# Kernel tuning notes

Measured on AMD Instinct MI355X. Metric: run time of the kernel, lower is better.

## Reference

```python
import jax, jax.numpy as jnp
import numpy as np

NUM_STEPS = 5


def setup_inputs() -> dict:
    key = jax.random.key(0)
    ks = jax.random.split(key, 12)
    B, N, H, E, A = 8, 1024, 64, 2, 8
    initial_state = jax.random.normal(ks[0], (B, N, H), dtype=jnp.float32)
    annotation = jax.random.normal(ks[1], (B, N, A), dtype=jnp.float32)
    # sparse-ish positive adjacency, scaled so matmul outputs don't saturate gates
    adj_matrix = jax.random.uniform(ks[2], (B, N, 2 * N * E), dtype=jnp.float32) * 0.01
    s = 0.05
    W_edge = jax.random.normal(ks[3], (H, H * E), dtype=jnp.float32) * s
    b_edge = jax.random.normal(ks[4], (H * E,), dtype=jnp.float32) * s
    W_gate = jax.random.normal(ks[5], (3 * H, H), dtype=jnp.float32) * s
    b_gate = jax.random.normal(ks[6], (H,), dtype=jnp.float32) * s
    W_hid = jax.random.normal(ks[7], (H + A, H), dtype=jnp.float32) * s
    b_hid = jax.random.normal(ks[8], (H,), dtype=jnp.float32) * s
    W_out = jax.random.normal(ks[9], (H, 1), dtype=jnp.float32) * s
    b_out = jax.random.normal(ks[10], (1,), dtype=jnp.float32) * s
    return dict(initial_state=initial_state, annotation=annotation, adj_matrix=adj_matrix,
                W_edge=W_edge, b_edge=b_edge, W_gate=W_gate, b_gate=b_gate,
                W_hid=W_hid, b_hid=b_hid, W_out=W_out, b_out=b_out)


def reference(initial_state, annotation, adj_matrix, W_edge, b_edge,
              W_gate, b_gate, W_hid, b_hid, W_out, b_out):
    B, N, H = initial_state.shape
    E = W_edge.shape[1] // H
    boundary = N * E
    A_in = adj_matrix[:, :, :boundary]   # [B, N, N*E]
    A_out = adj_matrix[:, :, boundary:]  # [B, N, N*E]

    h = initial_state
    for _ in range(NUM_STEPS):
        # Linear(H, H*E) then view/transpose to [B, N*E, H].
        # Original computes incoming_edge and outgoing_edge with the SAME
        # linear on the SAME input -> identical tensors; compute once.
        edge = jnp.einsum('bnh,he->bne', h, W_edge) + b_edge      # [B, N, H*E]
        edge = edge.reshape(B, N, H, E).transpose(0, 3, 1, 2).reshape(B, N * E, H)
        a_in = jnp.matmul(A_in, edge)    # [B, N, H]
        a_out = jnp.matmul(A_out, edge)  # [B, N, H]
        a = jnp.concatenate([a_in, a_out, h], axis=2)             # [B, N, 3H]
        # update and reset use the same gate linear -> equal; compute once.
        z = jax.nn.sigmoid(jnp.einsum('bnk,kh->bnh', a, W_gate) + b_gate)
        a_r = jnp.concatenate([a_in, a_out, z * h], axis=2)
        h_tilde = jnp.tanh(jnp.einsum('bnk,kh->bnh', a_r, W_gate) + b_gate)
        h = (1.0 - z) * h + z * h_tilde

    # task_id not in {18, 19}: node-level output head
    ha = jnp.concatenate([h, annotation], axis=2)                 # [B, N, H+A]
    out = jnp.tanh(jnp.einsum('bnk,kh->bnh', ha, W_hid) + b_hid)  # [B, N, H]
    out = (jnp.einsum('bnh,ho->bno', out, W_out) + b_out).sum(axis=2)  # [B, N]
    return out
```

## Files before the change

### kernel.cpp

```cpp
#include <hip/hip_runtime.h>
#include <math.h>

#define BN    8
#define NN    1024
#define HH    64
#define ADIM  8
#define STEPS 5
#define K2    2048
#define ROWS  (BN*NN)

typedef __attribute__((ext_vector_type(8))) short bf16x8;
typedef __attribute__((ext_vector_type(4))) float f32x4;

__device__ __forceinline__ unsigned short f2bf(float f) {
    unsigned int u = __float_as_uint(f);
    u += 0x7FFF + ((u >> 16) & 1);
    return (unsigned short)(u >> 16);
}
__device__ __forceinline__ float bf2f(unsigned short h) {
    return __uint_as_float(((unsigned int)h) << 16);
}

__global__ __launch_bounds__(256) void conv_adj(
    const float* __restrict__ in, unsigned short* __restrict__ out)
{
    int tid = blockIdx.x * 256 + threadIdx.x;
    #pragma unroll
    for (int i = 0; i < 4; ++i) {
        size_t idx = (size_t)tid + (size_t)i * 2097152;
        float4 v = ((const float4*)in)[idx];
        ushort4 o;
        o.x = f2bf(v.x); o.y = f2bf(v.y); o.z = f2bf(v.z); o.w = f2bf(v.w);
        ((ushort4*)out)[idx] = o;
    }
}

__global__ __launch_bounds__(256) void prep_pack(
    const float* __restrict__ Wg, const float* __restrict__ We,
    unsigned short* __restrict__ wgp, unsigned short* __restrict__ wep)
{
    int t = blockIdx.x * 256 + threadIdx.x;
    if (t < 12288) {
        int k = t >> 6, c = t & 63;
        float v = Wg[t];
        unsigned short hi = f2bf(v);
        unsigned short lo = f2bf(v - bf2f(hi));
        wgp[(size_t)c * 192 + k] = hi;
        wgp[(size_t)(64 + c) * 192 + k] = lo;
    } else if (t < 20480) {
        int u = t - 12288;
        int k = u >> 7, c = u & 127;
        float v = We[u];
        unsigned short hi = f2bf(v);
        unsigned short lo = f2bf(v - bf2f(hi));
        wep[(size_t)c * 64 + k] = hi;
        wep[(size_t)(128 + c) * 64 + k] = lo;
    }
}

__global__ __launch_bounds__(256) void init_kernel(
    const float* __restrict__ init_state,
    const float* __restrict__ We, const float* __restrict__ be,
    float* __restrict__ h_ws, unsigned short* __restrict__ edge_t)
{
    __shared__ float h_lds[4][65];
    int t = threadIdx.x;
    int r = t >> 6, hp = t & 63;
    int row = blockIdx.x * 4 + r;
    float hv = init_state[(size_t)row * 64 + hp];
    h_ws[(size_t)row * 64 + hp] = hv;
    h_lds[r][hp] = hv;
    __syncthreads();
    int b = row >> 10, n = row & 1023;
    #pragma unroll
    for (int e = 0; e < 2; ++e) {
        float acc = be[hp * 2 + e];
        #pragma unroll 8
        for (int c = 0; c < 64; ++c)
            acc += h_lds[r][c] * We[c * 128 + hp * 2 + e];
        edge_t[((size_t)b * 64 + hp) * K2 + e * NN + n] = f2bf(acc);
    }
}

__global__ __launch_bounds__(256) void step_kernel(
    const unsigned short* __restrict__ adjb,
    const unsigned short* __restrict__ ein,
    unsigned short* __restrict__ eout,
    float* __restrict__ h_ws,
    const unsigned short* __restrict__ wgp,
    const unsigned short* __restrict__ wep,
    const float* __restrict__ bg,
    const float* __restrict__ be,
    int do_edge)
{
    __shared__ __attribute__((aligned(16))) unsigned short Bs[2][64][264];
    __shared__ __attribute__((aligned(16))) unsigned short Xhi[32][200];
    __shared__ __attribute__((aligned(16))) unsigned short Xlo[32][200];
    __shared__ __attribute__((aligned(16))) float          hf [32][68];
    __shared__ __attribute__((aligned(16))) unsigned short HNhi[32][72];
    __shared__ __attribute__((aligned(16))) unsigned short HNlo[32][72];

    int t  = threadIdx.x;
    int b  = blockIdx.x >> 5;
    int mt = blockIdx.x & 31;
    int n0 = mt * 32;
    size_t hbase = ((size_t)(b * NN + n0)) * 64;

    {
        int r = t >> 3, cg = (t & 7) * 8;
        const float* hptr = h_ws + hbase + (size_t)r * 64 + cg;
        float4 v0 = *(const float4*)hptr;
        float4 v1 = *(const float4*)(hptr + 4);
        float vv[8] = {v0.x, v0.y, v0.z, v0.w, v1.x, v1.y, v1.z, v1.w};
        #pragma unroll
        for (int j = 0; j < 8; ++j) {
            float v = vv[j];
            unsigned short hi = f2bf(v), lo = f2bf(v - bf2f(hi));
            Xhi[r][128 + cg + j] = hi;
            Xlo[r][128 + cg + j] = lo;
            hf[r][cg + j] = v;
        }
    }

    int lane = t & 63, w = t >> 6, l15 = lane & 15, q = lane >> 4;
    int dir = w >> 1, rh = w & 1;

    const unsigned short* Abase = adjb
        + ((size_t)(b * NN + n0 + rh * 16 + l15)) * 4096 + dir * K2;

    int srow[8], scol[8];
    const unsigned short* sptr[8];
    #pragma unroll
    for (int i = 0; i < 8; ++i) {
        int u = i * 256 + t;
        srow[i] = u >> 5; scol[i] = (u & 31) * 8;
        sptr[i] = ein + ((size_t)b * 64 + srow[i]) * K2 + scol[i];
    }
    #pragma unroll
    for (int i = 0; i < 8; ++i)
        *(uint4*)&Bs[0][srow[i]][scol[i]] = *(const uint4*)(sptr[i]);
    __syncthreads();

    f32x4 acc[4];
    #pragma unroll
    for (int ct = 0; ct < 4; ++ct) acc[ct] = (f32x4){0.f, 0.f, 0.f, 0.f};

    bf16x8 af[8];
    #pragma unroll
    for (int ks = 0; ks < 8; ++ks)
        af[ks] = *(const bf16x8*)(Abase + ks * 32 + q * 8);

    #pragma unroll
    for (int c = 0; c < 8; ++c) {
        int buf = c & 1;
        uint4 g[8];
        bf16x8 afn[8];
        if (c < 7) {
            #pragma unroll
            for (int i = 0; i < 8; ++i)
                g[i] = *(const uint4*)(sptr[i] + (c + 1) * 256);
            #pragma unroll
            for (int ks = 0; ks < 8; ++ks)
                afn[ks] = *(const bf16x8*)(Abase + (c + 1) * 256 + ks * 32 + q * 8);
        }
        #pragma unroll
        for (int ks = 0; ks < 8; ++ks) {
            #pragma unroll
            for (int ct = 0; ct < 4; ++ct) {
                bf16x8 bfr = *(const bf16x8*)&Bs[buf][ct * 16 + l15][ks * 32 + q * 8];
                acc[ct] = __builtin_amdgcn_mfma_f32_16x16x32_bf16(af[ks], bfr, acc[ct], 0, 0, 0);
            }
        }
        if (c < 7) {
            #pragma unroll
            for (int i = 0; i < 8; ++i)
                *(uint4*)&Bs[buf ^ 1][srow[i]][scol[i]] = g[i];
            #pragma unroll
            for (int ks = 0; ks < 8; ++ks) af[ks] = afn[ks];
        }
        __syncthreads();
    }

    #pragma unroll
    for (int ct = 0; ct < 4; ++ct) {
        #pragma unroll
        for (int i = 0; i < 4; ++i) {
            float v = acc[ct][i];
            unsigned short hi = f2bf(v), lo = f2bf(v - bf2f(hi));
            int r  = rh * 16 + q * 4 + i;
            int cc = dir * 64 + ct * 16 + l15;
            Xhi[r][cc] = hi;
            Xlo[r][cc] = lo;
        }
    }
    __syncthreads();

    int mg = w & 1, ct0 = (w >> 1) * 2;
    int arow = mg * 16 + l15;
    f32x4 as[2], az[2];
    as[0] = as[1] = (f32x4){0.f, 0.f, 0.f, 0.f};

    #pragma unroll
    for (int ks = 0; ks < 4; ++ks) {
        bf16x8 ah = *(const bf16x8*)&Xhi[arow][ks * 32 + q * 8];
        bf16x8 al = *(const bf16x8*)&Xlo[arow][ks * 32 + q * 8];
        #pragma unroll
        for (int p = 0; p < 2; ++p) {
            int cc = (ct0 + p) * 16 + l15;
            const unsigned short* wb = wgp + (size_t)cc * 192 + ks * 32 + q * 8;
            bf16x8 bh = *(const bf16x8*)wb;
            bf16x8 bl = *(const bf16x8*)(wb + 64 * 192);
            as[p] = __builtin_amdgcn_mfma_f32_16x16x32_bf16(ah, bh, as[p], 0, 0, 0);
            as[p] = __builtin_amdgcn_mfma_f32_16x16x32_bf16(ah, bl, as[p], 0, 0, 0);
            as[p] = __builtin_amdgcn_mfma_f32_16x16x32_bf16(al, bh, as[p], 0, 0, 0);
        }
    }
    az[0] = as[0]; az[1] = as[1];
    #pragma unroll
    for (int ks = 4; ks < 6; ++ks) {
        bf16x8 ah = *(const bf16x8*)&Xhi[arow][ks * 32 + q * 8];
        bf16x8 al = *(const bf16x8*)&Xlo[arow][ks * 32 + q * 8];
        #pragma unroll
        for (int p = 0; p < 2; ++p) {
            int cc = (ct0 + p) * 16 + l15;
            const unsigned short* wb = wgp + (size_t)cc * 192 + ks * 32 + q * 8;
            bf16x8 bh = *(const bf16x8*)wb;
            bf16x8 bl = *(const bf16x8*)(wb + 64 * 192);
            az[p] = __builtin_amdgcn_mfma_f32_16x16x32_bf16(ah, bh, az[p], 0, 0, 0);
            az[p] = __builtin_amdgcn_mfma_f32_16x16x32_bf16(ah, bl, az[p], 0, 0, 0);
            az[p] = __builtin_amdgcn_mfma_f32_16x16x32_bf16(al, bh, az[p], 0, 0, 0);
        }
    }
    __syncthreads();

    float zv[2][4], hv[2][4];
    #pragma unroll
    for (int p = 0; p < 2; ++p) {
        int cc = (ct0 + p) * 16 + l15;
        float bgv = bg[cc];
        #pragma unroll
        for (int i = 0; i < 4; ++i) {
            int r = mg * 16 + q * 4 + i;
            float z = 1.f / (1.f + __expf(-(az[p][i] + bgv)));
            float h = hf[r][cc];
            zv[p][i] = z; hv[p][i] = h;
            float zh = z * h;
            unsigned short hi = f2bf(zh), lo = f2bf(zh - bf2f(hi));
            Xhi[r][128 + cc] = hi;
            Xlo[r][128 + cc] = lo;
        }
    }
    __syncthreads();

    #pragma unroll
    for (int ks = 4; ks < 6; ++ks) {
        bf16x8 ah = *(const bf16x8*)&Xhi[arow][ks * 32 + q * 8];
        bf16x8 al = *(const bf16x8*)&Xlo[arow][ks * 32 + q * 8];
        #pragma unroll
        for (int p = 0; p < 2; ++p) {
            int cc = (ct0 + p) * 16 + l15;
            const unsigned short* wb = wgp + (size_t)cc * 192 + ks * 32 + q * 8;
            bf16x8 bh = *(const bf16x8*)wb;
            bf16x8 bl = *(const bf16x8*)(wb + 64 * 192);
            as[p] = __builtin_amdgcn_mfma_f32_16x16x32_bf16(ah, bh, as[p], 0, 0, 0);
            as[p] = __builtin_amdgcn_mfma_f32_16x16x32_bf16(ah, bl, as[p], 0, 0, 0);
            as[p] = __builtin_amdgcn_mfma_f32_16x16x32_bf16(al, bh, as[p], 0, 0, 0);
        }
    }

    #pragma unroll
    for (int p = 0; p < 2; ++p) {
        int cc = (ct0 + p) * 16 + l15;
        float bgv = bg[cc];
        #pragma unroll
        for (int i = 0; i < 4; ++i) {
            int r = mg * 16 + q * 4 + i;
            float ht = tanhf(as[p][i] + bgv);
            float z  = zv[p][i];
            float hn = (1.f - z) * hv[p][i] + z * ht;
            h_ws[hbase + (size_t)r * 64 + cc] = hn;
            if (do_edge) {
                unsigned short hi = f2bf(hn), lo = f2bf(hn - bf2f(hi));
                HNhi[r][cc] = hi;
                HNlo[r][cc] = lo;
            }
        }
    }
    if (!do_edge) return;
    __syncthreads();

    int me = w & 1, cb = (w >> 1) * 4;
    int erow = me * 16 + l15;
    f32x4 ae[4];
    #pragma unroll
    for (int p = 0; p < 4; ++p) ae[p] = (f32x4){0.f, 0.f, 0.f, 0.f};
    #pragma unroll
    for (int ks = 0; ks < 2; ++ks) {
        bf16x8 ah = *(const bf16x8*)&HNhi[erow][ks * 32 + q * 8];
        bf16x8 al = *(const bf16x8*)&HNlo[erow][ks * 32 + q * 8];
        #pragma unroll
        for (int p = 0; p < 4; ++p) {
            int cc = (cb + p) * 16 + l15;
            const unsigned short* wb = wep + (size_t)cc * 64 + ks * 32 + q * 8;
            bf16x8 bh = *(const bf16x8*)wb;
            bf16x8 bl = *(const bf16x8*)(wb + 128 * 64);
            ae[p] = __builtin_amdgcn_mfma_f32_16x16x32_bf16(ah, bh, ae[p], 0, 0, 0);
            ae[p] = __builtin_amdgcn_mfma_f32_16x16x32_bf16(ah, bl, ae[p], 0, 0, 0);
            ae[p] = __builtin_amdgcn_mfma_f32_16x16x32_bf16(al, bh, ae[p], 0, 0, 0);
        }
    }
    #pragma unroll
    for (int p = 0; p < 4; ++p) {
        int cc = (cb + p) * 16 + l15;
        float bev = be[cc];
        int hp2 = cc >> 1, e = cc & 1;
        size_t ebase = ((size_t)b * 64 + hp2) * K2 + (size_t)e * NN
                     + n0 + me * 16 + q * 4;
        ushort4 ev;
        ev.x = f2bf(ae[p][0] + bev);
        ev.y = f2bf(ae[p][1] + bev);
        ev.z = f2bf(ae[p][2] + bev);
        ev.w = f2bf(ae[p][3] + bev);
        *(ushort4*)(eout + ebase) = ev;
    }
}

__global__ __launch_bounds__(256) void head_kernel(
    const float* __restrict__ h_ws, const float* __restrict__ ann,
    const float* __restrict__ Wh, const float* __restrict__ bh,
    const float* __restrict__ Wo, const float* __restrict__ bo,
    float* __restrict__ out)
{
    __shared__ float Wh_l[72 * 64];
    __shared__ float ha[4][72];
    int t = threadIdx.x;
    #pragma unroll
    for (int l = 0; l < 18; ++l) {
        int idx = t + l * 256;
        Wh_l[idx] = Wh[idx];
    }
    int r = t >> 6, hp = t & 63;
    int row = blockIdx.x * 4 + r;
    ha[r][hp] = h_ws[(size_t)row * 64 + hp];
    if (hp < ADIM) ha[r][64 + hp] = ann[(size_t)row * ADIM + hp];
    __syncthreads();

    float acc = bh[hp];
    #pragma unroll 8
    for (int k = 0; k < 72; ++k)
        acc += ha[r][k] * Wh_l[k * 64 + hp];
    float v = tanhf(acc) * Wo[hp];
    #pragma unroll
    for (int o = 32; o; o >>= 1) v += __shfl_down(v, o, 64);
    if (hp == 0) out[row] = v + bo[0];
}

extern "C" void kernel_launch(void* const* d_in, const int* in_sizes, int n_in,
                              void* d_out, int out_size, void* d_ws, size_t ws_size,
                              hipStream_t stream) {
    const float* init_state = (const float*)d_in[0];
    const float* ann = (const float*)d_in[1];
    const float* adj = (const float*)d_in[2];
    const float* We  = (const float*)d_in[3];
    const float* be  = (const float*)d_in[4];
    const float* Wg  = (const float*)d_in[5];
    const float* bg  = (const float*)d_in[6];
    const float* Wh  = (const float*)d_in[7];
    const float* bh  = (const float*)d_in[8];
    const float* Wo  = (const float*)d_in[9];
    const float* bo  = (const float*)d_in[10];
    float* out = (float*)d_out;

    char* wsb = (char*)d_ws;
    unsigned short* adj_bf = (unsigned short*)wsb;
    unsigned short* edge_a = (unsigned short*)(wsb + 67108864);
    unsigned short* edge_b = (unsigned short*)(wsb + 69206016);
    float*          h_ws   = (float*)(wsb + 71303168);
    unsigned short* wgp    = (unsigned short*)(wsb + 73400320);
    unsigned short* wep    = (unsigned short*)(wsb + 73449472);

    conv_adj<<<dim3(8192), dim3(256), 0, stream>>>(adj, adj_bf);
    prep_pack<<<dim3(80), dim3(256), 0, stream>>>(Wg, We, wgp, wep);
    init_kernel<<<dim3(ROWS / 4), dim3(256), 0, stream>>>(init_state, We, be, h_ws, edge_a);
    for (int s = 0; s < STEPS; ++s) {
        const unsigned short* ein = (s & 1) ? edge_b : edge_a;
        unsigned short* eo        = (s & 1) ? edge_a : edge_b;
        step_kernel<<<dim3(256), dim3(256), 0, stream>>>(
            adj_bf, ein, eo, h_ws, wgp, wep, bg, be, (s < STEPS - 1) ? 1 : 0);
    }
    head_kernel<<<dim3(ROWS / 4), dim3(256), 0, stream>>>(h_ws, ann, Wh, bh, Wo, bo, out);
}
```

Measured before the change: 381.0 us.

## Double step kernel threads with split-K across wave pairs and LDS reduction

The step kernel now runs 512 threads per block instead of 256. Each pair of waves splits the K range of every adjacency chunk and combines partial accumulators through an LDS reduction that reuses the B staging buffer. The gate and edge GEMMs are redistributed so each wave handles one column tile instead of two or four. The goal is more waves in flight to hide memory latency in a grid of only 256 blocks, at the cost of an extra reduction pass and barrier.

```diff
diff --git a/kernel.cpp b/kernel.cpp
--- a/kernel.cpp
+++ b/kernel.cpp
@@ -82,7 +82,7 @@
     }
 }
 
-__global__ __launch_bounds__(256) void step_kernel(
+__global__ __launch_bounds__(512) void step_kernel(
     const unsigned short* __restrict__ adjb,
     const unsigned short* __restrict__ ein,
     unsigned short* __restrict__ eout,
@@ -107,37 +107,35 @@
     size_t hbase = ((size_t)(b * NN + n0)) * 64;
 
     {
-        int r = t >> 3, cg = (t & 7) * 8;
-        const float* hptr = h_ws + hbase + (size_t)r * 64 + cg;
-        float4 v0 = *(const float4*)hptr;
-        float4 v1 = *(const float4*)(hptr + 4);
-        float vv[8] = {v0.x, v0.y, v0.z, v0.w, v1.x, v1.y, v1.z, v1.w};
-        #pragma unroll
-        for (int j = 0; j < 8; ++j) {
-            float v = vv[j];
-            unsigned short hi = f2bf(v), lo = f2bf(v - bf2f(hi));
+        int r = t >> 4, cg = (t & 15) * 4;
+        float4 v = *(const float4*)(h_ws + hbase + (size_t)r * 64 + cg);
+        float vv[4] = {v.x, v.y, v.z, v.w};
+        #pragma unroll
+        for (int j = 0; j < 4; ++j) {
+            float hv = vv[j];
+            unsigned short hi = f2bf(hv), lo = f2bf(hv - bf2f(hi));
             Xhi[r][128 + cg + j] = hi;
             Xlo[r][128 + cg + j] = lo;
-            hf[r][cg + j] = v;
+            hf[r][cg + j] = hv;
         }
     }
 
     int lane = t & 63, w = t >> 6, l15 = lane & 15, q = lane >> 4;
-    int dir = w >> 1, rh = w & 1;
+    int dir = w >> 2, rh = (w >> 1) & 1, kc = w & 1;
 
     const unsigned short* Abase = adjb
-        + ((size_t)(b * NN + n0 + rh * 16 + l15)) * 4096 + dir * K2;
-
-    int srow[8], scol[8];
-    const unsigned short* sptr[8];
-    #pragma unroll
-    for (int i = 0; i < 8; ++i) {
-        int u = i * 256 + t;
+        + ((size_t)(b * NN + n0 + rh * 16 + l15)) * 4096 + dir * K2 + kc * 128;
+
+    int srow[4], scol[4];
+    const unsigned short* sptr[4];
+    #pragma unroll
+    for (int i = 0; i < 4; ++i) {
+        int u = i * 512 + t;
         srow[i] = u >> 5; scol[i] = (u & 31) * 8;
         sptr[i] = ein + ((size_t)b * 64 + srow[i]) * K2 + scol[i];
     }
     #pragma unroll
-    for (int i = 0; i < 8; ++i)
+    for (int i = 0; i < 4; ++i)
         *(uint4*)&Bs[0][srow[i]][scol[i]] = *(const uint4*)(sptr[i]);
     __syncthreads();
 
@@ -145,110 +143,110 @@
     #pragma unroll
     for (int ct = 0; ct < 4; ++ct) acc[ct] = (f32x4){0.f, 0.f, 0.f, 0.f};
 
-    bf16x8 af[8];
-    #pragma unroll
-    for (int ks = 0; ks < 8; ++ks)
+    bf16x8 af[4];
+    #pragma unroll
+    for (int ks = 0; ks < 4; ++ks)
         af[ks] = *(const bf16x8*)(Abase + ks * 32 + q * 8);
 
     #pragma unroll
     for (int c = 0; c < 8; ++c) {
         int buf = c & 1;
-        uint4 g[8];
-        bf16x8 afn[8];
+        uint4 g[4];
+        bf16x8 afn[4];
         if (c < 7) {
             #pragma unroll
-            for (int i = 0; i < 8; ++i)
+            for (int i = 0; i < 4; ++i)
                 g[i] = *(const uint4*)(sptr[i] + (c + 1) * 256);
             #pragma unroll
-            for (int ks = 0; ks < 8; ++ks)
+            for (int ks = 0; ks < 4; ++ks)
                 afn[ks] = *(const bf16x8*)(Abase + (c + 1) * 256 + ks * 32 + q * 8);
         }
         #pragma unroll
-        for (int ks = 0; ks < 8; ++ks) {
+        for (int ks = 0; ks < 4; ++ks) {
             #pragma unroll
             for (int ct = 0; ct < 4; ++ct) {
-                bf16x8 bfr = *(const bf16x8*)&Bs[buf][ct * 16 + l15][ks * 32 + q * 8];
+                bf16x8 bfr = *(const bf16x8*)&Bs[buf][ct * 16 + l15][kc * 128 + ks * 32 + q * 8];
                 acc[ct] = __builtin_amdgcn_mfma_f32_16x16x32_bf16(af[ks], bfr, acc[ct], 0, 0, 0);
             }
         }
         if (c < 7) {
             #pragma unroll
-            for (int i = 0; i < 8; ++i)
+            for (int i = 0; i < 4; ++i)
                 *(uint4*)&Bs[buf ^ 1][srow[i]][scol[i]] = g[i];
             #pragma unroll
-            for (int ks = 0; ks < 8; ++ks) af[ks] = afn[ks];
+            for (int ks = 0; ks < 4; ++ks) af[ks] = afn[ks];
         }
         __syncthreads();
     }
 
-    #pragma unroll
-    for (int ct = 0; ct < 4; ++ct) {
-        #pragma unroll
-        for (int i = 0; i < 4; ++i) {
-            float v = acc[ct][i];
-            unsigned short hi = f2bf(v), lo = f2bf(v - bf2f(hi));
-            int r  = rh * 16 + q * 4 + i;
-            int cc = dir * 64 + ct * 16 + l15;
-            Xhi[r][cc] = hi;
-            Xlo[r][cc] = lo;
-        }
-    }
-    __syncthreads();
-
-    int mg = w & 1, ct0 = (w >> 1) * 2;
+    float (*red)[16][68] = (float (*)[16][68])(&Bs[0][0][0]);
+    int gg = w >> 1;
+    if (kc == 1) {
+        #pragma unroll
+        for (int ct = 0; ct < 4; ++ct)
+            #pragma unroll
+            for (int i = 0; i < 4; ++i)
+                red[gg][q * 4 + i][ct * 16 + l15] = acc[ct][i];
+    }
+    __syncthreads();
+    if (kc == 0) {
+        #pragma unroll
+        for (int ct = 0; ct < 4; ++ct)
+            #pragma unroll
+            for (int i = 0; i < 4; ++i) {
+                float v = acc[ct][i] + red[gg][q * 4 + i][ct * 16 + l15];
+                unsigned short hi = f2bf(v), lo = f2bf(v - bf2f(hi));
+                int r  = rh * 16 + q * 4 + i;
+                int cc = dir * 64 + ct * 16 + l15;
+                Xhi[r][cc] = hi;
+                Xlo[r][cc] = lo;
+            }
+    }
+    __syncthreads();
+
+    int mg = w & 1, cg16 = w >> 1;
     int arow = mg * 16 + l15;
-    f32x4 as[2], az[2];
-    as[0] = as[1] = (f32x4){0.f, 0.f, 0.f, 0.f};
+    int cc = cg16 * 16 + l15;
+    const unsigned short* wcol = wgp + (size_t)cc * 192;
+    f32x4 as = (f32x4){0.f, 0.f, 0.f, 0.f}, az;
 
     #pragma unroll
     for (int ks = 0; ks < 4; ++ks) {
         bf16x8 ah = *(const bf16x8*)&Xhi[arow][ks * 32 + q * 8];
         bf16x8 al = *(const bf16x8*)&Xlo[arow][ks * 32 + q * 8];
-        #pragma unroll
-        for (int p = 0; p < 2; ++p) {
-            int cc = (ct0 + p) * 16 + l15;
-            const unsigned short* wb = wgp + (size_t)cc * 192 + ks * 32 + q * 8;
-            bf16x8 bh = *(const bf16x8*)wb;
-            bf16x8 bl = *(const bf16x8*)(wb + 64 * 192);
-            as[p] = __builtin_amdgcn_mfma_f32_16x16x32_bf16(ah, bh, as[p], 0, 0, 0);
-            as[p] = __builtin_amdgcn_mfma_f32_16x16x32_bf16(ah, bl, as[p], 0, 0, 0);
-            as[p] = __builtin_amdgcn_mfma_f32_16x16x32_bf16(al, bh, as[p], 0, 0, 0);
-        }
-    }
-    az[0] = as[0]; az[1] = as[1];
+        const unsigned short* wb = wcol + ks * 32 + q * 8;
+        bf16x8 bh = *(const bf16x8*)wb;
+        bf16x8 bl = *(const bf16x8*)(wb + 64 * 192);
+        as = __builtin_amdgcn_mfma_f32_16x16x32_bf16(ah, bh, as, 0, 0, 0);
+        as = __builtin_amdgcn_mfma_f32_16x16x32_bf16(ah, bl, as, 0, 0, 0);
+        as = __builtin_amdgcn_mfma_f32_16x16x32_bf16(al, bh, as, 0, 0, 0);
+    }
+    az = as;
     #pragma unroll
     for (int ks = 4; ks < 6; ++ks) {
         bf16x8 ah = *(const bf16x8*)&Xhi[arow][ks * 32 + q * 8];
         bf16x8 al = *(const bf16x8*)&Xlo[arow][ks * 32 + q * 8];
-        #pragma unroll
-        for (int p = 0; p < 2; ++p) {
-            int cc = (ct0 + p) * 16 + l15;
-            const unsigned short* wb = wgp + (size_t)cc * 192 + ks * 32 + q * 8;
-            bf16x8 bh = *(const bf16x8*)wb;
-            bf16x8 bl = *(const bf16x8*)(wb + 64 * 192);
-            az[p] = __builtin_amdgcn_mfma_f32_16x16x32_bf16(ah, bh, az[p], 0, 0, 0);
-            az[p] = __builtin_amdgcn_mfma_f32_16x16x32_bf16(ah, bl, az[p], 0, 0, 0);
-            az[p] = __builtin_amdgcn_mfma_f32_16x16x32_bf16(al, bh, az[p], 0, 0, 0);
-        }
-    }
-    __syncthreads();
-
-    float zv[2][4], hv[2][4];
-    #pragma unroll
-    for (int p = 0; p < 2; ++p) {
-        int cc = (ct0 + p) * 16 + l15;
-        float bgv = bg[cc];
-        #pragma unroll
-        for (int i = 0; i < 4; ++i) {
-            int r = mg * 16 + q * 4 + i;
-            float z = 1.f / (1.f + __expf(-(az[p][i] + bgv)));
-            float h = hf[r][cc];
-            zv[p][i] = z; hv[p][i] = h;
-            float zh = z * h;
-            unsigned short hi = f2bf(zh), lo = f2bf(zh - bf2f(hi));
-            Xhi[r][128 + cc] = hi;
-            Xlo[r][128 + cc] = lo;
-        }
+        const unsigned short* wb = wcol + ks * 32 + q * 8;
+        bf16x8 bh = *(const bf16x8*)wb;
+        bf16x8 bl = *(const bf16x8*)(wb + 64 * 192);
+        az = __builtin_amdgcn_mfma_f32_16x16x32_bf16(ah, bh, az, 0, 0, 0);
+        az = __builtin_amdgcn_mfma_f32_16x16x32_bf16(ah, bl, az, 0, 0, 0);
+        az = __builtin_amdgcn_mfma_f32_16x16x32_bf16(al, bh, az, 0, 0, 0);
+    }
+    __syncthreads();
+
+    float zv[4], hv[4];
+    float bgv = bg[cc];
+    #pragma unroll
+    for (int i = 0; i < 4; ++i) {
+        int r = mg * 16 + q * 4 + i;
+        float z = 1.f / (1.f + __expf(-(az[i] + bgv)));
+        float h = hf[r][cc];
+        zv[i] = z; hv[i] = h;
+        float zh = z * h;
+        unsigned short hi = f2bf(zh), lo = f2bf(zh - bf2f(hi));
+        Xhi[r][128 + cc] = hi;
+        Xlo[r][128 + cc] = lo;
     }
     __syncthreads();
 
@@ -256,52 +254,42 @@
     for (int ks = 4; ks < 6; ++ks) {
         bf16x8 ah = *(const bf16x8*)&Xhi[arow][ks * 32 + q * 8];
         bf16x8 al = *(const bf16x8*)&Xlo[arow][ks * 32 + q * 8];
-        #pragma unroll
-        for (int p = 0; p < 2; ++p) {
-            int cc = (ct0 + p) * 16 + l15;
-            const unsigned short* wb = wgp + (size_t)cc * 192 + ks * 32 + q * 8;
-            bf16x8 bh = *(const bf16x8*)wb;
-            bf16x8 bl = *(const bf16x8*)(wb + 64 * 192);
-            as[p] = __builtin_amdgcn_mfma_f32_16x16x32_bf16(ah, bh, as[p], 0, 0, 0);
-            as[p] = __builtin_amdgcn_mfma_f32_16x16x32_bf16(ah, bl, as[p], 0, 0, 0);
-            as[p] = __builtin_amdgcn_mfma_f32_16x16x32_bf16(al, bh, as[p], 0, 0, 0);
-        }
-    }
-
-    #pragma unroll
-    for (int p = 0; p < 2; ++p) {
-        int cc = (ct0 + p) * 16 + l15;
-        float bgv = bg[cc];
-        #pragma unroll
-        for (int i = 0; i < 4; ++i) {
-            int r = mg * 16 + q * 4 + i;
-            float ht = tanhf(as[p][i] + bgv);
-            float z  = zv[p][i];
-            float hn = (1.f - z) * hv[p][i] + z * ht;
-            h_ws[hbase + (size_t)r * 64 + cc] = hn;
-            if (do_edge) {
-                unsigned short hi = f2bf(hn), lo = f2bf(hn - bf2f(hi));
-                HNhi[r][cc] = hi;
-                HNlo[r][cc] = lo;
-            }
+        const unsigned short* wb = wcol + ks * 32 + q * 8;
+        bf16x8 bh = *(const bf16x8*)wb;
+        bf16x8 bl = *(const bf16x8*)(wb + 64 * 192);
+        as = __builtin_amdgcn_mfma_f32_16x16x32_bf16(ah, bh, as, 0, 0, 0);
+        as = __builtin_amdgcn_mfma_f32_16x16x32_bf16(ah, bl, as, 0, 0, 0);
+        as = __builtin_amdgcn_mfma_f32_16x16x32_bf16(al, bh, as, 0, 0, 0);
+    }
+
+    #pragma unroll
+    for (int i = 0; i < 4; ++i) {
+        int r = mg * 16 + q * 4 + i;
+        float ht = tanhf(as[i] + bgv);
+        float z  = zv[i];
+        float hn = (1.f - z) * hv[i] + z * ht;
+        h_ws[hbase + (size_t)r * 64 + cc] = hn;
+        if (do_edge) {
+            unsigned short hi = f2bf(hn), lo = f2bf(hn - bf2f(hi));
+            HNhi[r][cc] = hi;
+            HNlo[r][cc] = lo;
         }
     }
     if (!do_edge) return;
     __syncthreads();
 
-    int me = w & 1, cb = (w >> 1) * 4;
+    int me = w & 1, cb2 = (w >> 1) * 2;
     int erow = me * 16 + l15;
-    f32x4 ae[4];
-    #pragma unroll
-    for (int p = 0; p < 4; ++p) ae[p] = (f32x4){0.f, 0.f, 0.f, 0.f};
+    f32x4 ae[2];
+    ae[0] = ae[1] = (f32x4){0.f, 0.f, 0.f, 0.f};
     #pragma unroll
     for (int ks = 0; ks < 2; ++ks) {
         bf16x8 ah = *(const bf16x8*)&HNhi[erow][ks * 32 + q * 8];
         bf16x8 al = *(const bf16x8*)&HNlo[erow][ks * 32 + q * 8];
         #pragma unroll
-        for (int p = 0; p < 4; ++p) {
-            int cc = (cb + p) * 16 + l15;
-            const unsigned short* wb = wep + (size_t)cc * 64 + ks * 32 + q * 8;
+        for (int p = 0; p < 2; ++p) {
+            int ec = (cb2 + p) * 16 + l15;
+            const unsigned short* wb = wep + (size_t)ec * 64 + ks * 32 + q * 8;
             bf16x8 bh = *(const bf16x8*)wb;
             bf16x8 bl = *(const bf16x8*)(wb + 128 * 64);
             ae[p] = __builtin_amdgcn_mfma_f32_16x16x32_bf16(ah, bh, ae[p], 0, 0, 0);
@@ -310,10 +298,10 @@
         }
     }
     #pragma unroll
-    for (int p = 0; p < 4; ++p) {
-        int cc = (cb + p) * 16 + l15;
-        float bev = be[cc];
-        int hp2 = cc >> 1, e = cc & 1;
+    for (int p = 0; p < 2; ++p) {
+        int ec = (cb2 + p) * 16 + l15;
+        float bev = be[ec];
+        int hp2 = ec >> 1, e = ec & 1;
         size_t ebase = ((size_t)b * 64 + hp2) * K2 + (size_t)e * NN
                      + n0 + me * 16 + q * 4;
         ushort4 ev;
@@ -385,7 +373,7 @@
     for (int s = 0; s < STEPS; ++s) {
         const unsigned short* ein = (s & 1) ? edge_b : edge_a;
         unsigned short* eo        = (s & 1) ? edge_a : edge_b;
-        step_kernel<<<dim3(256), dim3(256), 0, stream>>>(
+        step_kernel<<<dim3(256), dim3(512), 0, stream>>>(
             adj_bf, ein, eo, h_ws, wgp, wep, bg, be, (s < STEPS - 1) ? 1 : 0);
     }
     head_kernel<<<dim3(ROWS / 4), dim3(256), 0, stream>>>(h_ws, ann, Wh, bh, Wo, bo, out);
```

Result: no change. 384.1 us (+0.8%).
